# Kernel optimization log

Measured on AMD Instinct MI355X. Metric: run time of the kernel, lower is better.

The kernel has to match this reference:

```python
import jax, jax.numpy as jnp
import numpy as np

B, S, DIM = 2, 2048, 4096
NH, NKV, HD = 32, 8, 128  # q heads, kv heads, head dim
ROPE_THETA = 10000.0


def _rope_tables(seq_len, head_dim, dtype=jnp.float32):
    inv = 1.0 / (ROPE_THETA ** (jnp.arange(0, head_dim, 2, dtype=jnp.float32) / head_dim))
    t = jnp.arange(seq_len, dtype=jnp.float32)
    f = jnp.outer(t, inv)  # [S, HD/2]
    return jnp.cos(f).astype(dtype), jnp.sin(f).astype(dtype)


def setup_inputs() -> dict:
    key = jax.random.key(0)
    ks = jax.random.split(key, 5)
    cos, sin = _rope_tables(S, HD)
    scale = 0.02
    return {
        "x": jax.random.normal(ks[0], (B, S, DIM), jnp.float32),
        "start_pos": 0,
        "freqs_cos": cos,
        "freqs_sin": sin,
        "wq": jax.random.normal(ks[1], (DIM, NH * HD), jnp.float32) * scale,
        "wk": jax.random.normal(ks[2], (DIM, NKV * HD), jnp.float32) * scale,
        "wv": jax.random.normal(ks[3], (DIM, NKV * HD), jnp.float32) * scale,
        "wo": jax.random.normal(ks[4], (NH * HD, DIM), jnp.float32) * scale,
    }


def _apply_rope(x, cos, sin):
    # x: [B, S, H, D]; rotate interleaved (even, odd) pairs as complex numbers
    xr, xi = x[..., 0::2], x[..., 1::2]
    c = cos[None, :, None, :]
    s = sin[None, :, None, :]
    out_r = xr * c - xi * s
    out_i = xr * s + xi * c
    return jnp.stack([out_r, out_i], axis=-1).reshape(x.shape)


def reference(x, start_pos, freqs_cos, freqs_sin, wq, wk, wv, wo):
    b, s, _ = x.shape
    n_rep = NH // NKV
    xq = (x @ wq).reshape(b, s, NH, HD)
    xk = (x @ wk).reshape(b, s, NKV, HD)
    xv = (x @ wv).reshape(b, s, NKV, HD)
    xq = _apply_rope(xq, freqs_cos, freqs_sin)
    xk = _apply_rope(xk, freqs_cos, freqs_sin)
    # GQA: group q heads [B,S,NKV,n_rep,HD] against shared kv heads (no repeat_kv materialization)
    xqg = xq.reshape(b, s, NKV, n_rep, HD)
    scale = 1.0 / jnp.sqrt(jnp.asarray(HD, x.dtype))
    scores = jnp.einsum('bqhrd,bkhd->bhrqk', xqg, xk) * scale  # [B,NKV,n_rep,S,S]
    probs = jax.nn.softmax(scores, axis=-1)
    out = jnp.einsum('bhrqk,bkhd->bqhrd', probs, xv)  # [B,S,NKV,n_rep,HD]
    out = out.reshape(b, s, NH * HD)
    return out @ wo
```

## Files before the change

### kernel.cpp

```cpp
#include <hip/hip_runtime.h>

typedef unsigned short u16;
typedef unsigned int   u32;
typedef __attribute__((ext_vector_type(4))) float floatx4;
typedef __attribute__((ext_vector_type(8))) short shortx8;
typedef __attribute__((ext_vector_type(8))) u16   ushortx8;

#define B_   2
#define S_   2048
#define DIM_ 4096
#define NH_  32
#define NKV_ 8
#define HD_  128
#define MTOT (B_*S_)
#define NQKV (NH_*HD_ + 2*NKV_*HD_)
#define QSCALE 0.08838834764831845f

__device__ inline u16 f2bf(float f) {
  u32 x = __builtin_bit_cast(u32, f);
  x += 0x7fffu + ((x >> 16) & 1u);
  return (u16)(x >> 16);
}
__device__ inline float bf2f(u16 u) {
  u32 x = ((u32)u) << 16;
  return __builtin_bit_cast(float, x);
}
__device__ inline shortx8 ldfrag(const u16* p) {
  return __builtin_bit_cast(shortx8, *(const uint4*)p);
}

__global__ __launch_bounds__(256) void cvt_f32_bf16(const float* __restrict__ src,
                                                    u16* __restrict__ dst) {
  int i = blockIdx.x * 256 + threadIdx.x;
  const float4* s4 = (const float4*)src;
  float4 a = s4[2*i], c = s4[2*i+1];
  ushortx8 o;
  o[0]=f2bf(a.x); o[1]=f2bf(a.y); o[2]=f2bf(a.z); o[3]=f2bf(a.w);
  o[4]=f2bf(c.x); o[5]=f2bf(c.y); o[6]=f2bf(c.z); o[7]=f2bf(c.w);
  *(ushortx8*)(dst + (size_t)i*8) = o;
}

__global__ __launch_bounds__(256) void transpose_cvt(const float* __restrict__ w,
                                                     u16* __restrict__ wt, int K, int N) {
  __shared__ float tile[32][33];
  int n0 = blockIdx.x * 32, k0 = blockIdx.y * 32;
  int tx = threadIdx.x & 31, ty = threadIdx.x >> 5;
#pragma unroll
  for (int i = 0; i < 4; i++) {
    int r = ty*4 + i;
    tile[r][tx] = w[(size_t)(k0 + r)*N + n0 + tx];
  }
  __syncthreads();
#pragma unroll
  for (int i = 0; i < 4; i++) {
    int n = ty*4 + i;
    wt[(size_t)(n0 + n)*K + k0 + tx] = f2bf(tile[tx][n]);
  }
}

template<int OUT_BF16>
__global__ __launch_bounds__(256) void gemm_bt(const u16* __restrict__ A,
                                               const u16* __restrict__ Bt,
                                               void* __restrict__ Cv,
                                               int M, int N, int K) {
  __shared__ u16 As[128*72];
  __shared__ u16 Bs[128*72];
  const int tid = threadIdx.x;
  const int w = tid >> 6, l = tid & 63, quad = l >> 4, c16 = l & 15;
  const int bm = blockIdx.y * 128, bn = blockIdx.x * 128;
  const int wm = (w & 1) * 64, wn = (w >> 1) * 64;
  floatx4 acc[4][4];
#pragma unroll
  for (int mi = 0; mi < 4; mi++)
#pragma unroll
    for (int ni = 0; ni < 4; ni++) acc[mi][ni] = floatx4{0.f,0.f,0.f,0.f};

  for (int k0 = 0; k0 < K; k0 += 64) {
    __syncthreads();
#pragma unroll
    for (int rep = 0; rep < 4; rep++) {
      int c = rep*256 + tid;
      int r = c >> 3, cc = c & 7;
      uint4 va = *(const uint4*)(A  + (size_t)(bm + r)*K + k0 + cc*8);
      uint4 vb = *(const uint4*)(Bt + (size_t)(bn + r)*K + k0 + cc*8);
      *(uint4*)(As + r*72 + cc*8) = va;
      *(uint4*)(Bs + r*72 + cc*8) = vb;
    }
    __syncthreads();
#pragma unroll
    for (int ks = 0; ks < 2; ks++) {
      shortx8 af[4], bfr[4];
#pragma unroll
      for (int mi = 0; mi < 4; mi++)
        af[mi] = ldfrag(As + (wm + mi*16 + c16)*72 + ks*32 + quad*8);
#pragma unroll
      for (int ni = 0; ni < 4; ni++)
        bfr[ni] = ldfrag(Bs + (wn + ni*16 + c16)*72 + ks*32 + quad*8);
#pragma unroll
      for (int mi = 0; mi < 4; mi++)
#pragma unroll
        for (int ni = 0; ni < 4; ni++)
          acc[mi][ni] = __builtin_amdgcn_mfma_f32_16x16x32_bf16(af[mi], bfr[ni], acc[mi][ni], 0, 0, 0);
    }
  }
#pragma unroll
  for (int mi = 0; mi < 4; mi++)
#pragma unroll
    for (int i = 0; i < 4; i++) {
      int row = bm + wm + mi*16 + quad*4 + i;
#pragma unroll
      for (int ni = 0; ni < 4; ni++) {
        int col = bn + wn + ni*16 + c16;
        float v = acc[mi][ni][i];
        if (OUT_BF16) ((u16*)Cv)[(size_t)row*N + col] = f2bf(v);
        else          ((float*)Cv)[(size_t)row*N + col] = v;
      }
    }
}

__global__ __launch_bounds__(256) void rope_kernel(const u16* __restrict__ qkv,
                                                   const float* __restrict__ fc,
                                                   const float* __restrict__ fs,
                                                   u16* __restrict__ q_r,
                                                   u16* __restrict__ k_r) {
  u32 idx  = blockIdx.x * 256 + threadIdx.x;
  u32 t    = idx & 63;
  u32 rest = idx >> 6;
  u32 m    = rest / 40u;
  u32 hh   = rest - m*40u;
  u32 s    = m & (S_ - 1);
  float c  = fc[s*64 + t], sn = fs[s*64 + t];
  u32 src; u16* dst; u32 dstoff; float scale;
  if (hh < (u32)NH_) {
    src = m*NQKV + hh*HD_ + 2*t;  dst = q_r;  dstoff = m*(NH_*HD_) + hh*HD_ + 2*t;  scale = QSCALE;
  } else {
    u32 hk = hh - NH_;
    src = m*NQKV + NH_*HD_ + hk*HD_ + 2*t;  dst = k_r;  dstoff = m*(NKV_*HD_) + hk*HD_ + 2*t;  scale = 1.f;
  }
  u32 pair = *(const u32*)(qkv + src);
  float xr = bf2f((u16)(pair & 0xffffu));
  float xi = bf2f((u16)(pair >> 16));
  float orr = (xr*c - xi*sn) * scale;
  float oii = (xr*sn + xi*c) * scale;
  u32 outp = (u32)f2bf(orr) | ((u32)f2bf(oii) << 16);
  *(u32*)(dst + dstoff) = outp;
}

__global__ __launch_bounds__(256) void v_transpose(const u16* __restrict__ qkv,
                                                   u16* __restrict__ vt) {
  __shared__ u16 tile[32][33];
  int bh = blockIdx.y; int b = bh >> 3, hk = bh & 7;
  int ts = (blockIdx.x & 63) * 32;
  int td = (blockIdx.x >> 6) * 32;
  int tx = threadIdx.x & 31, ty = threadIdx.x >> 5;
#pragma unroll
  for (int i = 0; i < 4; i++) {
    int r = ty*4 + i;
    tile[r][tx] = qkv[(size_t)(b*S_ + ts + r)*NQKV + (NH_*HD_ + NKV_*HD_) + hk*HD_ + td + tx];
  }
  __syncthreads();
#pragma unroll
  for (int i = 0; i < 4; i++) {
    int d = ty*4 + i;
    vt[((size_t)bh*HD_ + td + d)*S_ + ts + tx] = tile[tx][d];
  }
}

__global__ __launch_bounds__(256) void attn_kernel(const u16* __restrict__ Q,
                                                   const u16* __restrict__ Kr,
                                                   const u16* __restrict__ Vt,
                                                   u16* __restrict__ Out) {
  __shared__ u16 Qs[64*136];
  __shared__ u16 Ks[64*136];
  __shared__ u16 Vts[128*72];
  __shared__ u16 Ps[4*16*72];
  const int tid = threadIdx.x;
  const int w = tid >> 6, l = tid & 63, quad = l >> 4, c16 = l & 15;
  const int qt = blockIdx.x, h = blockIdx.y, b = blockIdx.z;
  const int hk = h >> 2;

#pragma unroll
  for (int rep = 0; rep < 4; rep++) {
    int c = rep*256 + tid;
    int r = c >> 4, cc = c & 15;
    uint4 v = *(const uint4*)(Q + (size_t)(b*S_ + qt*64 + r)*(NH_*HD_) + h*HD_ + cc*8);
    *(uint4*)(Qs + r*136 + cc*8) = v;
  }
  __syncthreads();
  shortx8 aq[4];
#pragma unroll
  for (int kk = 0; kk < 4; kk++)
    aq[kk] = ldfrag(Qs + (w*16 + c16)*136 + kk*32 + quad*8);

  floatx4 o[8];
#pragma unroll
  for (int f = 0; f < 8; f++) o[f] = floatx4{0.f,0.f,0.f,0.f};
  float mrow[4] = {-1e30f,-1e30f,-1e30f,-1e30f};
  float lrow[4] = {0.f,0.f,0.f,0.f};
  u16* pw = Ps + w*16*72;

  for (int kt = 0; kt < S_/64; kt++) {
    __syncthreads();
#pragma unroll
    for (int rep = 0; rep < 4; rep++) {
      int c = rep*256 + tid;
      int r = c >> 4, cc = c & 15;
      uint4 v = *(const uint4*)(Kr + (size_t)(b*S_ + kt*64 + r)*(NKV_*HD_) + hk*HD_ + cc*8);
      *(uint4*)(Ks + r*136 + cc*8) = v;
      int d = c >> 3, cc2 = c & 7;
      uint4 v2 = *(const uint4*)(Vt + ((size_t)(b*NKV_ + hk)*HD_ + d)*S_ + kt*64 + cc2*8);
      *(uint4*)(Vts + d*72 + cc2*8) = v2;
    }
    __syncthreads();

    floatx4 sc[4];
#pragma unroll
    for (int nt = 0; nt < 4; nt++) sc[nt] = floatx4{0.f,0.f,0.f,0.f};
#pragma unroll
    for (int kk = 0; kk < 4; kk++)
#pragma unroll
      for (int nt = 0; nt < 4; nt++) {
        shortx8 bk = ldfrag(Ks + (nt*16 + c16)*136 + kk*32 + quad*8);
        sc[nt] = __builtin_amdgcn_mfma_f32_16x16x32_bf16(aq[kk], bk, sc[nt], 0, 0, 0);
      }

    float alpha[4];
#pragma unroll
    for (int i = 0; i < 4; i++) {
      float mx = fmaxf(fmaxf(sc[0][i], sc[1][i]), fmaxf(sc[2][i], sc[3][i]));
      mx = fmaxf(mx, __shfl_xor(mx, 1));
      mx = fmaxf(mx, __shfl_xor(mx, 2));
      mx = fmaxf(mx, __shfl_xor(mx, 4));
      mx = fmaxf(mx, __shfl_xor(mx, 8));
      float mn = fmaxf(mrow[i], mx);
      float al = __expf(mrow[i] - mn);
      mrow[i] = mn;
      float rs = 0.f;
#pragma unroll
      for (int nt = 0; nt < 4; nt++) { float p = __expf(sc[nt][i] - mn); sc[nt][i] = p; rs += p; }
      rs += __shfl_xor(rs, 1);
      rs += __shfl_xor(rs, 2);
      rs += __shfl_xor(rs, 4);
      rs += __shfl_xor(rs, 8);
      lrow[i] = lrow[i]*al + rs;
      alpha[i] = al;
    }
#pragma unroll
    for (int f = 0; f < 8; f++)
#pragma unroll
      for (int i = 0; i < 4; i++) o[f][i] *= alpha[i];

#pragma unroll
    for (int nt = 0; nt < 4; nt++)
#pragma unroll
      for (int i = 0; i < 4; i++)
        pw[(quad*4 + i)*72 + nt*16 + c16] = f2bf(sc[nt][i]);
    asm volatile("s_waitcnt lgkmcnt(0)" ::: "memory");

#pragma unroll
    for (int kk2 = 0; kk2 < 2; kk2++) {
      shortx8 pf = ldfrag(pw + c16*72 + kk2*32 + quad*8);
#pragma unroll
      for (int f = 0; f < 8; f++) {
        shortx8 vf = ldfrag(Vts + (f*16 + c16)*72 + kk2*32 + quad*8);
        o[f] = __builtin_amdgcn_mfma_f32_16x16x32_bf16(pf, vf, o[f], 0, 0, 0);
      }
    }
  }

#pragma unroll
  for (int i = 0; i < 4; i++) {
    int srow = qt*64 + w*16 + quad*4 + i;
    float inv = 1.f / lrow[i];
    size_t base = (size_t)(b*S_ + srow)*(NH_*HD_) + h*HD_;
#pragma unroll
    for (int f = 0; f < 8; f++)
      Out[base + f*16 + c16] = f2bf(o[f][i] * inv);
  }
}

extern "C" void kernel_launch(void* const* d_in, const int* in_sizes, int n_in,
                              void* d_out, int out_size, void* d_ws, size_t ws_size,
                              hipStream_t stream) {
  (void)in_sizes; (void)n_in; (void)out_size; (void)ws_size;
  const float* x  = (const float*)d_in[0];
  const float* fc = (const float*)d_in[2];
  const float* fs = (const float*)d_in[3];
  const float* wq = (const float*)d_in[4];
  const float* wk = (const float*)d_in[5];
  const float* wv = (const float*)d_in[6];
  const float* wo = (const float*)d_in[7];
  float* out = (float*)d_out;

  char* ws = (char*)d_ws;
  u16* xb    = (u16*)(ws);
  u16* wallt = (u16*)(ws + 33554432ull);
  u16* q_r   = (u16*)(ws + 33554432ull);
  u16* k_r   = (u16*)(ws + 67108864ull);
  u16* vt    = (u16*)(ws + 75497472ull);
  u16* wot   = (u16*)(ws + 83886080ull);
  u16* qkvp  = (u16*)(ws + 117440512ull);

  cvt_f32_bf16<<<8192, 256, 0, stream>>>(x, xb);
  transpose_cvt<<<dim3(128,128), 256, 0, stream>>>(wq, wallt, 4096, 4096);
  transpose_cvt<<<dim3(32,128),  256, 0, stream>>>(wk, wallt + (size_t)4096*4096, 4096, 1024);
  transpose_cvt<<<dim3(32,128),  256, 0, stream>>>(wv, wallt + (size_t)5120*4096, 4096, 1024);
  transpose_cvt<<<dim3(128,128), 256, 0, stream>>>(wo, wot, 4096, 4096);

  gemm_bt<1><<<dim3(48,32), 256, 0, stream>>>(xb, wallt, qkvp, MTOT, NQKV, DIM_);

  rope_kernel<<<40960, 256, 0, stream>>>(qkvp, fc, fs, q_r, k_r);
  v_transpose<<<dim3(256,16), 256, 0, stream>>>(qkvp, vt);

  attn_kernel<<<dim3(32,32,2), 256, 0, stream>>>(q_r, k_r, vt, xb);

  gemm_bt<0><<<dim3(32,32), 256, 0, stream>>>(xb, wot, out, MTOT, DIM_, 4096);
}
```

Before: 1.079 ms.

## Use direct global-to-LDS loads in GEMM, exp2 softmax, reuse Q LDS for P

The GEMM tile loads now use global_load_lds to write straight into unpadded LDS, skipping the register round trip, at the cost of possible bank conflicts from dropping the padding. Softmax switches to the hardware exp2 instruction, with log2(e) folded into the Q scale. The P staging buffer is aliased onto the Q shared buffer to cut LDS use and raise occupancy. f2bf now uses the compiler's native bf16 conversion.

```diff
diff --git a/kernel.cpp b/kernel.cpp
--- a/kernel.cpp
+++ b/kernel.cpp
@@ -14,12 +14,15 @@
 #define HD_  128
 #define MTOT (B_*S_)
 #define NQKV (NH_*HD_ + 2*NKV_*HD_)
-#define QSCALE 0.08838834764831845f
+#define QSCALE 0.12753785735803168f
+#define KSCALE 1.0f
+
+typedef __attribute__((address_space(3))) u32 lds_u32;
+typedef const __attribute__((address_space(1))) u32 gbl_u32;
 
 __device__ inline u16 f2bf(float f) {
-  u32 x = __builtin_bit_cast(u32, f);
-  x += 0x7fffu + ((x >> 16) & 1u);
-  return (u16)(x >> 16);
+  __bf16 h = (__bf16)f;
+  return __builtin_bit_cast(u16, h);
 }
 __device__ inline float bf2f(u16 u) {
   u32 x = ((u32)u) << 16;
@@ -63,12 +66,14 @@
                                                const u16* __restrict__ Bt,
                                                void* __restrict__ Cv,
                                                int M, int N, int K) {
-  __shared__ u16 As[128*72];
-  __shared__ u16 Bs[128*72];
+  __shared__ u16 As[128*64];
+  __shared__ u16 Bs[128*64];
   const int tid = threadIdx.x;
   const int w = tid >> 6, l = tid & 63, quad = l >> 4, c16 = l & 15;
   const int bm = blockIdx.y * 128, bn = blockIdx.x * 128;
   const int wm = (w & 1) * 64, wn = (w >> 1) * 64;
+  const int drow = l >> 3;
+  const int dcol = (l & 7) * 8;
   floatx4 acc[4][4];
 #pragma unroll
   for (int mi = 0; mi < 4; mi++)
@@ -78,13 +83,14 @@
   for (int k0 = 0; k0 < K; k0 += 64) {
     __syncthreads();
 #pragma unroll
-    for (int rep = 0; rep < 4; rep++) {
-      int c = rep*256 + tid;
-      int r = c >> 3, cc = c & 7;
-      uint4 va = *(const uint4*)(A  + (size_t)(bm + r)*K + k0 + cc*8);
-      uint4 vb = *(const uint4*)(Bt + (size_t)(bn + r)*K + k0 + cc*8);
-      *(uint4*)(As + r*72 + cc*8) = va;
-      *(uint4*)(Bs + r*72 + cc*8) = vb;
+    for (int j = 0; j < 4; j++) {
+      int row = w*32 + j*8 + drow;
+      __builtin_amdgcn_global_load_lds(
+          (gbl_u32*)(A + (size_t)(bm + row)*K + k0 + dcol),
+          (lds_u32*)(As + (w*32 + j*8)*64), 16, 0, 0);
+      __builtin_amdgcn_global_load_lds(
+          (gbl_u32*)(Bt + (size_t)(bn + row)*K + k0 + dcol),
+          (lds_u32*)(Bs + (w*32 + j*8)*64), 16, 0, 0);
     }
     __syncthreads();
 #pragma unroll
@@ -92,10 +98,10 @@
       shortx8 af[4], bfr[4];
 #pragma unroll
       for (int mi = 0; mi < 4; mi++)
-        af[mi] = ldfrag(As + (wm + mi*16 + c16)*72 + ks*32 + quad*8);
+        af[mi] = ldfrag(As + (wm + mi*16 + c16)*64 + ks*32 + quad*8);
 #pragma unroll
       for (int ni = 0; ni < 4; ni++)
-        bfr[ni] = ldfrag(Bs + (wn + ni*16 + c16)*72 + ks*32 + quad*8);
+        bfr[ni] = ldfrag(Bs + (wn + ni*16 + c16)*64 + ks*32 + quad*8);
 #pragma unroll
       for (int mi = 0; mi < 4; mi++)
 #pragma unroll
@@ -135,7 +141,7 @@
     src = m*NQKV + hh*HD_ + 2*t;  dst = q_r;  dstoff = m*(NH_*HD_) + hh*HD_ + 2*t;  scale = QSCALE;
   } else {
     u32 hk = hh - NH_;
-    src = m*NQKV + NH_*HD_ + hk*HD_ + 2*t;  dst = k_r;  dstoff = m*(NKV_*HD_) + hk*HD_ + 2*t;  scale = 1.f;
+    src = m*NQKV + NH_*HD_ + hk*HD_ + 2*t;  dst = k_r;  dstoff = m*(NKV_*HD_) + hk*HD_ + 2*t;  scale = KSCALE;
   }
   u32 pair = *(const u32*)(qkv + src);
   float xr = bf2f((u16)(pair & 0xffffu));
@@ -173,7 +179,6 @@
   __shared__ u16 Qs[64*136];
   __shared__ u16 Ks[64*136];
   __shared__ u16 Vts[128*72];
-  __shared__ u16 Ps[4*16*72];
   const int tid = threadIdx.x;
   const int w = tid >> 6, l = tid & 63, quad = l >> 4, c16 = l & 15;
   const int qt = blockIdx.x, h = blockIdx.y, b = blockIdx.z;
@@ -197,7 +202,7 @@
   for (int f = 0; f < 8; f++) o[f] = floatx4{0.f,0.f,0.f,0.f};
   float mrow[4] = {-1e30f,-1e30f,-1e30f,-1e30f};
   float lrow[4] = {0.f,0.f,0.f,0.f};
-  u16* pw = Ps + w*16*72;
+  u16* pw = Qs + w*16*72;
 
   for (int kt = 0; kt < S_/64; kt++) {
     __syncthreads();
@@ -233,11 +238,14 @@
       mx = fmaxf(mx, __shfl_xor(mx, 4));
       mx = fmaxf(mx, __shfl_xor(mx, 8));
       float mn = fmaxf(mrow[i], mx);
-      float al = __expf(mrow[i] - mn);
+      float al = __builtin_amdgcn_exp2f(mrow[i] - mn);
       mrow[i] = mn;
       float rs = 0.f;
 #pragma unroll
-      for (int nt = 0; nt < 4; nt++) { float p = __expf(sc[nt][i] - mn); sc[nt][i] = p; rs += p; }
+      for (int nt = 0; nt < 4; nt++) {
+        float p = __builtin_amdgcn_exp2f(sc[nt][i] - mn);
+        sc[nt][i] = p; rs += p;
+      }
       rs += __shfl_xor(rs, 1);
       rs += __shfl_xor(rs, 2);
       rs += __shfl_xor(rs, 4);
```

Measured after the change: 1.077 ms. Within noise of the previous version (-0.2%).
